# Performance work log

Hardware: AMD Instinct MI355X
Metric: run time of the kernel (lower is better)

Reference implementation:

```python
import jax, jax.numpy as jnp
import numpy as np

N_DRUG, N_TARGET, N_EDGES, H = 50000, 20000, 500000, 256


def setup_inputs() -> dict:
    key = jax.random.key(0)
    ks = jax.random.split(key, 6)
    s = 1.0 / np.sqrt(2 * H)
    return {
        "z_drug": jax.random.normal(ks[0], (N_DRUG, H), dtype=jnp.float32),
        "z_target": jax.random.normal(ks[1], (N_TARGET, H), dtype=jnp.float32),
        "row": jax.random.randint(ks[2], (N_EDGES,), 0, N_DRUG, dtype=jnp.int64),
        "col": jax.random.randint(ks[3], (N_EDGES,), 0, N_TARGET, dtype=jnp.int64),
        "W1": jax.random.normal(ks[4], (2 * H, H), dtype=jnp.float32) * s,
        "b1": jnp.zeros((H,), dtype=jnp.float32),
        "W2": jax.random.normal(ks[5], (H, 1), dtype=jnp.float32) * (1.0 / np.sqrt(H)),
        "b2": jnp.zeros((1,), dtype=jnp.float32),
    }


def reference(z_drug, z_target, row, col, W1, b1, W2, b2):
    # gather endpoint embeddings by edge index, concat -> [E, 2H]
    zc = jnp.concatenate([z_drug[row], z_target[col]], axis=-1)
    h = jax.nn.relu(zc @ W1 + b1)          # [E, H]
    return h @ W2 + b2                     # [E, 1]
```

## Files before the change

kernel.cpp:

```cpp
#include <hip/hip_runtime.h>
#include <hip/hip_bf16.h>
#include <stdint.h>


typedef unsigned short u16;
typedef __attribute__((ext_vector_type(8))) short short8;
typedef __attribute__((ext_vector_type(4))) float f32x4;

#define HDIM 256
#define KDIM 512
#define BM 64
#define BK 64
#define NKC 8

__device__ __forceinline__ u16 f2bf(float f) {
  union { float f; uint32_t u; } v; v.f = f;
  uint32_t u = v.u;
  return (u16)((u + 0x7fffu + ((u >> 16) & 1u)) >> 16);
}

__device__ __forceinline__ void gl2lds16(const void* g, void* l) {
  __builtin_amdgcn_global_load_lds(
      (const __attribute__((address_space(1))) unsigned int*)g,
      (__attribute__((address_space(3))) unsigned int*)l,
      16, 0, 0);
}

#define CVT_BLOCKS 4096
__global__ void prep_kernel(const float* __restrict__ zd_f,
                            const float* __restrict__ zt_f,
                            const float* __restrict__ w1,
                            u16* __restrict__ zdb, u16* __restrict__ ztb,
                            u16* __restrict__ w1t, int n4d, int n4t) {
  const int b = blockIdx.x;
  if (b < 32) {
    __shared__ float tile[64][65];
    const int k0 = (b >> 2) * 64, n0 = (b & 3) * 64;
    const int tx = threadIdx.x & 63, ty = threadIdx.x >> 6;
#pragma unroll
    for (int i = ty; i < 64; i += 4)
      tile[i][tx] = w1[(size_t)(k0 + i) * HDIM + n0 + tx];
    __syncthreads();
#pragma unroll
    for (int i = ty; i < 64; i += 4)
      w1t[(size_t)(n0 + i) * KDIM + k0 + tx] = f2bf(tile[tx][i]);
  } else {
    const int idx = (b - 32) * 256 + threadIdx.x;
    const int stride = CVT_BLOCKS * 256;
    for (int i = idx; i < n4d; i += stride) {
      float4 v = ((const float4*)zd_f)[i];
      ushort4 o; o.x = f2bf(v.x); o.y = f2bf(v.y); o.z = f2bf(v.z); o.w = f2bf(v.w);
      ((ushort4*)zdb)[i] = o;
    }
    for (int i = idx; i < n4t; i += stride) {
      float4 v = ((const float4*)zt_f)[i];
      ushort4 o; o.x = f2bf(v.x); o.y = f2bf(v.y); o.z = f2bf(v.z); o.w = f2bf(v.w);
      ((ushort4*)ztb)[i] = o;
    }
  }
}

__global__ __launch_bounds__(256, 3) void edge_mlp_kernel(
    const u16* __restrict__ zd, const u16* __restrict__ zt,
    const int* __restrict__ row, const int* __restrict__ col,
    const u16* __restrict__ w1t, const float* __restrict__ b1,
    const float* __restrict__ w2, const float* __restrict__ b2,
    float* __restrict__ out, int E) {
  __shared__ u16 lA[2][BM * BK];
  __shared__ u16 lB[HDIM * BK];
  __shared__ float lP[4][BM];

  const int tid   = threadIdx.x;
  const int wid   = tid >> 6;
  const int lane  = tid & 63;
  const int colid = lane & 15;
  const int quad  = lane >> 4;
  const int e0    = blockIdx.x * BM;
  const int r8    = lane >> 3;
  const int slog  = ((lane & 7) ^ (r8 & 7)) * 8;
  const int csw   = colid & 7;

  const int eA = wid * 16 + r8;
  const int g1 = min(e0 + eA, E - 1);
  const int g2 = min(e0 + eA + 8, E - 1);
  const u16* pD1 = zd + (size_t)row[g1] * HDIM + slog;
  const u16* pT1 = zt + (size_t)col[g1] * HDIM + slog;
  const u16* pD2 = zd + (size_t)row[g2] * HDIM + slog;
  const u16* pT2 = zt + (size_t)col[g2] * HDIM + slog;
  const u16* pB = w1t + (size_t)(wid * 64 + r8) * KDIM + slog;

  f32x4 acc[4][4];
#pragma unroll
  for (int i = 0; i < 4; ++i)
#pragma unroll
    for (int j = 0; j < 4; ++j) acc[i][j] = f32x4{0.f, 0.f, 0.f, 0.f};

#define DMA_A(kc, buf)                                                         \
  {                                                                            \
    const int koff = ((kc) & 3) * BK;                                          \
    const u16* s1 = ((kc) < 4) ? (pD1 + koff) : (pT1 + koff);                  \
    const u16* s2 = ((kc) < 4) ? (pD2 + koff) : (pT2 + koff);                  \
    gl2lds16(s1, &lA[buf][(wid * 16) * BK]);                                   \
    gl2lds16(s2, &lA[buf][(wid * 16 + 8) * BK]);                               \
  }

  DMA_A(0, 0);

#pragma unroll
  for (int kc = 0; kc < NKC; ++kc) {
    __syncthreads();
#pragma unroll
    for (int j = 0; j < 8; ++j)
      gl2lds16(pB + (size_t)j * 8 * KDIM + kc * BK, &lB[(wid * 64 + j * 8) * BK]);
    __syncthreads();

    if (kc + 1 < NKC) DMA_A(kc + 1, (kc + 1) & 1);

    const u16* la = &lA[kc & 1][0];
#pragma unroll
    for (int ks = 0; ks < BK; ks += 32) {
      const int sl = (ks >> 3) + quad;
      short8 aF[4], bF[4];
#pragma unroll
      for (int rt = 0; rt < 4; ++rt)
        aF[rt] = *(const short8*)&la[(rt * 16 + colid) * BK + ((sl ^ csw) * 8)];
#pragma unroll
      for (int ct = 0; ct < 4; ++ct)
        bF[ct] = *(const short8*)&lB[(wid * 64 + ct * 16 + colid) * BK +
                                     ((sl ^ csw) * 8)];
#pragma unroll
      for (int rt = 0; rt < 4; ++rt)
#pragma unroll
        for (int ct = 0; ct < 4; ++ct)
          acc[rt][ct] = __builtin_amdgcn_mfma_f32_16x16x32_bf16(
              aF[rt], bF[ct], acc[rt][ct], 0, 0, 0);
    }
  }

  float b1v[4], w2v[4];
#pragma unroll
  for (int ct = 0; ct < 4; ++ct) {
    int n = wid * 64 + ct * 16 + colid;
    b1v[ct] = b1[n];
    w2v[ct] = w2[n];
  }
#pragma unroll
  for (int rt = 0; rt < 4; ++rt)
#pragma unroll
    for (int j = 0; j < 4; ++j) {
      float s = 0.f;
#pragma unroll
      for (int ct = 0; ct < 4; ++ct)
        s += fmaxf(acc[rt][ct][j] + b1v[ct], 0.f) * w2v[ct];
#pragma unroll
      for (int off = 8; off >= 1; off >>= 1)
        s += __shfl_xor(s, off, 16);
      if (colid == 0) lP[wid][rt * 16 + quad * 4 + j] = s;
    }
  __syncthreads();
  if (tid < BM) {
    int ge = e0 + tid;
    if (ge < E)
      out[ge] = lP[0][tid] + lP[1][tid] + lP[2][tid] + lP[3][tid] + b2[0];
  }
}

__global__ void fallback_kernel(
    const float* __restrict__ zd, const float* __restrict__ zt,
    const int* __restrict__ row, const int* __restrict__ col,
    const float* __restrict__ W1, const float* __restrict__ b1,
    const float* __restrict__ W2, const float* __restrict__ b2,
    float* __restrict__ out, int E) {
  __shared__ float zc[16][512];
  __shared__ float red[4][16];
  const int e0 = blockIdx.x * 16;
  const int tid = threadIdx.x;
  for (int i = tid; i < 16 * 512; i += 256) {
    int e = i >> 9, k = i & 511;
    int ge = min(e0 + e, E - 1);
    zc[e][k] = (k < HDIM) ? zd[(size_t)row[ge] * HDIM + k]
                          : zt[(size_t)col[ge] * HDIM + (k - HDIM)];
  }
  __syncthreads();
  float acc[16];
#pragma unroll
  for (int e = 0; e < 16; ++e) acc[e] = 0.f;
  for (int k = 0; k < KDIM; ++k) {
    float w = W1[k * HDIM + tid];
#pragma unroll
    for (int e = 0; e < 16; ++e) acc[e] += zc[e][k] * w;
  }
  float wv = W2[tid], bv = b1[tid];
  const int lane = tid & 63, wid = tid >> 6;
#pragma unroll
  for (int e = 0; e < 16; ++e) {
    float pv = fmaxf(acc[e] + bv, 0.f) * wv;
#pragma unroll
    for (int off = 32; off >= 1; off >>= 1) pv += __shfl_down(pv, off, 64);
    if (lane == 0) red[wid][e] = pv;
  }
  __syncthreads();
  if (tid < 16) {
    int ge = e0 + tid;
    if (ge < E)
      out[ge] = red[0][tid] + red[1][tid] + red[2][tid] + red[3][tid] + b2[0];
  }
}

extern "C" void kernel_launch(void* const* d_in, const int* in_sizes, int n_in,
                              void* d_out, int out_size, void* d_ws, size_t ws_size,
                              hipStream_t stream) {
  const float* zd_f = (const float*)d_in[0];
  const float* zt_f = (const float*)d_in[1];
  const int*   row  = (const int*)d_in[2];
  const int*   col  = (const int*)d_in[3];
  const float* W1   = (const float*)d_in[4];
  const float* b1   = (const float*)d_in[5];
  const float* W2   = (const float*)d_in[6];
  const float* b2   = (const float*)d_in[7];
  float* out = (float*)d_out;

  const int E  = in_sizes[2];
  const int ND = in_sizes[0] / HDIM;
  const int NT = in_sizes[1] / HDIM;

  size_t off_w1t = 0;
  size_t off_zd  = (size_t)KDIM * HDIM * sizeof(u16);
  size_t off_zt  = off_zd + (size_t)ND * HDIM * sizeof(u16);
  size_t need    = off_zt + (size_t)NT * HDIM * sizeof(u16);

  if (ws_size >= need) {
    u16* w1t = (u16*)((char*)d_ws + off_w1t);
    u16* zdb = (u16*)((char*)d_ws + off_zd);
    u16* ztb = (u16*)((char*)d_ws + off_zt);
    int n4d = ND * HDIM / 4, n4t = NT * HDIM / 4;
    prep_kernel<<<32 + CVT_BLOCKS, 256, 0, stream>>>(zd_f, zt_f, W1,
                                                     zdb, ztb, w1t, n4d, n4t);
    edge_mlp_kernel<<<(E + BM - 1) / BM, 256, 0, stream>>>(
        zdb, ztb, row, col, w1t, b1, W2, b2, out, E);
  } else {
    fallback_kernel<<<(E + 15) / 16, 256, 0, stream>>>(
        zd_f, zt_f, row, col, W1, b1, W2, b2, out, E);
  }
}
```

Measured before the change: 283.1 us.

## Double-buffer W1 tiles in LDS and use one barrier per K-chunk

Gives the W1 (B) tile its own double buffer alongside the gathered-edge (A) tile, in one flat shared array. The next chunk of both A and B is prefetched before computing the current chunk, so there is one barrier per iteration instead of two, and the W1 load no longer stalls the MFMA loop. The cost is more LDS per block (about 80 KB), so launch bounds drop from 3 to 2 blocks per CU. The final partial-sum buffer reuses the same shared memory.

```diff
diff --git a/kernel.cpp b/kernel.cpp
--- a/kernel.cpp
+++ b/kernel.cpp
@@ -60,15 +60,13 @@
   }
 }
 
-__global__ __launch_bounds__(256, 3) void edge_mlp_kernel(
+__global__ __launch_bounds__(256, 2) void edge_mlp_kernel(
     const u16* __restrict__ zd, const u16* __restrict__ zt,
     const int* __restrict__ row, const int* __restrict__ col,
     const u16* __restrict__ w1t, const float* __restrict__ b1,
     const float* __restrict__ w2, const float* __restrict__ b2,
     float* __restrict__ out, int E) {
-  __shared__ u16 lA[2][BM * BK];
-  __shared__ u16 lB[HDIM * BK];
-  __shared__ float lP[4][BM];
+  __shared__ u16 smem[40960];
 
   const int tid   = threadIdx.x;
   const int wid   = tid >> 6;
@@ -100,23 +98,29 @@
     const int koff = ((kc) & 3) * BK;                                          \
     const u16* s1 = ((kc) < 4) ? (pD1 + koff) : (pT1 + koff);                  \
     const u16* s2 = ((kc) < 4) ? (pD2 + koff) : (pT2 + koff);                  \
-    gl2lds16(s1, &lA[buf][(wid * 16) * BK]);                                   \
-    gl2lds16(s2, &lA[buf][(wid * 16 + 8) * BK]);                               \
+    gl2lds16(s1, &smem[(buf) * 4096 + (wid * 16) * BK]);                       \
+    gl2lds16(s2, &smem[(buf) * 4096 + (wid * 16 + 8) * BK]);                   \
+  }
+
+#define DMA_B(kc, buf)                                                         \
+  {                                                                            \
+    u16* dstb = &smem[8192 + (buf) * 16384 + (wid * 64) * BK];                 \
+    _Pragma("unroll") for (int j = 0; j < 8; ++j)                              \
+        gl2lds16(pB + (size_t)j * 8 * KDIM + (kc) * BK, dstb + j * 8 * BK);    \
   }
 
   DMA_A(0, 0);
+  DMA_B(0, 0);
+  __syncthreads();
 
 #pragma unroll
   for (int kc = 0; kc < NKC; ++kc) {
-    __syncthreads();
-#pragma unroll
-    for (int j = 0; j < 8; ++j)
-      gl2lds16(pB + (size_t)j * 8 * KDIM + kc * BK, &lB[(wid * 64 + j * 8) * BK]);
-    __syncthreads();
-
-    if (kc + 1 < NKC) DMA_A(kc + 1, (kc + 1) & 1);
-
-    const u16* la = &lA[kc & 1][0];
+    if (kc + 1 < NKC) {
+      DMA_A(kc + 1, (kc + 1) & 1);
+      DMA_B(kc + 1, (kc + 1) & 1);
+    }
+    const u16* la = &smem[(kc & 1) * 4096];
+    const u16* lb = &smem[8192 + (kc & 1) * 16384];
 #pragma unroll
     for (int ks = 0; ks < BK; ks += 32) {
       const int sl = (ks >> 3) + quad;
@@ -126,7 +130,7 @@
         aF[rt] = *(const short8*)&la[(rt * 16 + colid) * BK + ((sl ^ csw) * 8)];
 #pragma unroll
       for (int ct = 0; ct < 4; ++ct)
-        bF[ct] = *(const short8*)&lB[(wid * 64 + ct * 16 + colid) * BK +
+        bF[ct] = *(const short8*)&lb[(wid * 64 + ct * 16 + colid) * BK +
                                      ((sl ^ csw) * 8)];
 #pragma unroll
       for (int rt = 0; rt < 4; ++rt)
@@ -135,8 +139,10 @@
           acc[rt][ct] = __builtin_amdgcn_mfma_f32_16x16x32_bf16(
               aF[rt], bF[ct], acc[rt][ct], 0, 0, 0);
     }
-  }
-
+    __syncthreads();
+  }
+
+  float* lP = (float*)smem;
   float b1v[4], w2v[4];
 #pragma unroll
   for (int ct = 0; ct < 4; ++ct) {
@@ -155,13 +161,13 @@
 #pragma unroll
       for (int off = 8; off >= 1; off >>= 1)
         s += __shfl_xor(s, off, 16);
-      if (colid == 0) lP[wid][rt * 16 + quad * 4 + j] = s;
+      if (colid == 0) lP[wid * 64 + rt * 16 + quad * 4 + j] = s;
     }
   __syncthreads();
   if (tid < BM) {
     int ge = e0 + tid;
     if (ge < E)
-      out[ge] = lP[0][tid] + lP[1][tid] + lP[2][tid] + lP[3][tid] + b2[0];
+      out[ge] = lP[tid] + lP[64 + tid] + lP[128 + tid] + lP[192 + tid] + b2[0];
   }
 }
 
```

After: 304.0 us. 1.07x slower.
